# Kernel tuning notes

Measured on AMD Instinct MI355X. Metric: run time of the kernel, lower is better.

Reference implementation:

```python
import jax, jax.numpy as jnp
import numpy as np
import math

G = 256            # grid points per axis
L = 25.6           # cubic cell edge (bohr)
A = L / G          # grid spacing = 0.1 bohr
R_O = 2.0          # radial cutoff (bohr)
RMAX = int(math.ceil(R_O / A))   # 20
D = 2 * RMAX + 1                 # 41 box points per axis
N_ATOMS = 32
N_RAD = 4
N_L = 4
V_CELL = A ** 3
FOUR_PI = 4.0 * math.pi


def _make_W(n_rad):
    # NeuralXC ortho basis: S_ij = sqrt((5+2i)(5+2j))/(5+i+j), W = sqrtm(inv(S))
    i = np.arange(n_rad)
    S = np.sqrt((5.0 + 2 * i)[:, None] * (5.0 + 2 * i)[None, :]) / (5.0 + i[:, None] + i[None, :])
    w, V = np.linalg.eigh(np.linalg.inv(S))
    return (V * np.sqrt(w)) @ V.T


def setup_inputs():
    key = jax.random.key(0)
    k1, k2 = jax.random.split(key)
    rho = jax.random.uniform(k1, (G, G, G), dtype=jnp.float32)
    positions = jax.random.uniform(k2, (N_ATOMS, 3), dtype=jnp.float32) * L
    W = jnp.asarray(_make_W(N_RAD), dtype=jnp.float32)
    # periodic mesh offsets: [0..RMAX, -RMAX..-1] as in mesh_3d
    offs = jnp.concatenate([jnp.arange(0, RMAX + 1), jnp.arange(-RMAX, 0)]).astype(jnp.int32)
    return {"rho": rho, "positions": positions, "W": W, "offs": offs}


def _assoc_legendre(n_l, x, s):
    # P[l][m] for 0 <= m <= l < n_l, with Condon-Shortley phase
    P = [[None] * n_l for _ in range(n_l)]
    P[0][0] = jnp.ones_like(x)
    for m in range(n_l):
        if m > 0:
            P[m][m] = -(2 * m - 1) * s * P[m - 1][m - 1]
        if m + 1 < n_l:
            P[m + 1][m] = (2 * m + 1) * x * P[m][m]
        for l in range(m + 2, n_l):
            P[l][m] = ((2 * l - 1) * x * P[l - 1][m] - (l - 1 + m) * P[l - 2][m]) / (l - m)
    return P


def _real_sph_stack(n_l, theta, phi):
    # real spherical harmonics stacked in (l, m=-l..l) order -> [n_l**2, ...]
    x = jnp.cos(theta)
    s = jnp.sin(theta)
    P = _assoc_legendre(n_l, x, s)
    sq2 = math.sqrt(2.0)
    Ys = []
    for l in range(n_l):
        for m in range(-l, l + 1):
            am = abs(m)
            N = math.sqrt((2 * l + 1) / FOUR_PI * math.factorial(l - am) / math.factorial(l + am))
            if m == 0:
                Ys.append(N * P[l][0] * jnp.ones_like(x))
            elif m > 0:
                Ys.append(sq2 * ((-1) ** m) * N * P[l][m] * jnp.cos(m * phi))
            else:
                Ys.append(sq2 * ((-1) ** am) * N * P[l][am] * jnp.sin(am * phi))
    return jnp.stack(Ys)


def _radials(R, W):
    # g_a(r) = r^2 (r_o - r)^(a+2) / N_a for r < r_o, orthonormalized with W
    gs = []
    for a in range(N_RAD):
        Nn = math.sqrt(720.0 * R_O ** (11 + 2 * a) / float(np.prod([2 * a + k for k in range(5, 12)])))
        g = R ** 2 * (R_O - R) ** (a + 2) / Nn
        gs.append(jnp.where(R < R_O, g, 0.0))
    return jnp.einsum('nm,mxyz->nxyz', W, jnp.stack(gs))


def _project_atom(rho, pos, W, offs):
    cm = jnp.round(pos / A)                     # U_inv @ pos for diagonal cell
    dr = pos - A * cm
    idx = jnp.mod(offs[None, :] + cm.astype(jnp.int32)[:, None], G)   # [3, D] PBC mesh indices
    # separable irregular gather of the atom box (== torch rho[Xm,Ym,Zm] with fmod+negative-index wrap)
    srho = rho[idx[0][:, None, None], idx[1][None, :, None], idx[2][None, None, :]]  # [D,D,D]
    coord = A * offs.astype(jnp.float32)
    Xs = (coord - dr[0])[:, None, None]
    Ys = (coord - dr[1])[None, :, None]
    Zs = (coord - dr[2])[None, None, :]
    R = jnp.sqrt(Xs ** 2 + Ys ** 2 + Zs ** 2)   # [D,D,D]
    phi = jnp.arctan2(Ys, Xs)                   # [D,D,1], broadcasts
    small = R < 1e-15
    ratio = jnp.clip(jnp.where(small, 1.0, Zs / jnp.where(small, 1.0, R)), -1.0, 1.0)
    theta = jnp.where(small, 0.0, jnp.arccos(ratio))
    angs = _real_sph_stack(N_L, theta, phi)     # [N_L**2, D,D,D]
    rads = _radials(R, W) * V_CELL              # [N_RAD,  D,D,D]
    # equals the original padded 'lmijk,nijk,ijk->nlm' einsum followed by selecting |m|<=l,
    # flattened in (n, l, m) order
    coeff = jnp.einsum('cxyz,nxyz,xyz->nc', angs, rads, srho)
    return coeff.reshape(-1)                    # [N_RAD * N_L**2]


def reference(rho, positions, W, offs):
    return jax.vmap(lambda p: _project_atom(rho, p, W, offs))(positions)  # [N_ATOMS, 64]
```

## Files before the change

### kernel.cpp

```cpp
#include <hip/hip_runtime.h>
#include <math.h>

#define G 256
#define NATOMS 32
#define RC2I 435
#define NCHUNK 16

typedef float f32x2 __attribute__((ext_vector_type(2)));

struct PMap {
    int n;
    unsigned int pts[40960];
};

constexpr PMap make_pmap() {
    PMap m{};
    int p = 0;
    for (int i = 0; i < 41; ++i) {
        int di = i - 20;
        int mi = RC2I - di * di;
        for (int j = 0; j < 41; ++j) {
            int dj = j - 20;
            int mj = mi - dj * dj;
            if (mj >= 0) {
                int h = 0;
                while ((h + 1) * (h + 1) <= mj) ++h;
                for (int k = 20 - h; k <= 20 + h; ++k)
                    m.pts[p++] = (unsigned)(i | (j << 8) | (k << 16));
            }
        }
    }
    m.n = p;
    return m;
}

constexpr PMap h_pmap = make_pmap();
constexpr int NPTS = h_pmap.n;
__device__ const PMap d_pmap = h_pmap;

__global__ __launch_bounds__(256, 2) void proj_kernel(
    const float* __restrict__ rho,
    const float* __restrict__ positions,
    const float* __restrict__ W,
    float* __restrict__ out,
    float cs0, float cs1, float cs2, float cs3)
{
    const int atom = blockIdx.y;
    const int chunk = blockIdx.x;
    const int tid = threadIdx.x;
    const float A = 0.1f;

    __shared__ float red[256];

    float px = positions[atom * 3 + 0];
    float py = positions[atom * 3 + 1];
    float pz = positions[atom * 3 + 2];
    float cmx = rintf(px / A), cmy = rintf(py / A), cmz = rintf(pz / A);
    float drx = px - A * cmx, dry = py - A * cmy, drz = pz - A * cmz;
    int cxi = (int)cmx, cyi = (int)cmy, czi = (int)cmz;

    const int cxo = (cxi - 20) & 255;
    const int cyo = (cyi - 20) & 255;
    const int czo = (czi - 20) & 255;
    const float xoff = -2.0f - drx;
    const float yoff = -2.0f - dry;
    const float zoff = -2.0f - drz;

    const int pbeg = (chunk * NPTS) / NCHUNK;
    const int pend = ((chunk + 1) * NPTS) / NCHUNK;
    const unsigned int* __restrict__ pts = d_pmap.pts;

    f32x2 acc2[32];
#pragma unroll
    for (int q = 0; q < 32; ++q) acc2[q] = (f32x2){0.0f, 0.0f};

    for (int p = pbeg + tid; p < pend; p += 256) {
        unsigned pr = pts[p];
        int ii = pr & 255;
        int dj = (pr >> 8) & 255;
        int dk = pr >> 16;
        float srho = rho[(((ii + cxo) & 255) << 16) |
                         (((dj + cyo) & 255) << 8) |
                         ((dk + czo) & 255)];
        float Xd = fmaf(A, (float)ii, xoff);
        float Yd = fmaf(A, (float)dj, yoff);
        float Zd = fmaf(A, (float)dk, zoff);

        float r2 = fmaf(Xd, Xd, fmaf(Yd, Yd, Zd * Zd));
        float invr = rsqrtf(fmaxf(r2, 1e-24f));
        float r = r2 * invr;
        float t = fmaxf(2.0f - r, 0.0f);
        float tt = t * t;
        float rs = r2 * srho;
        float g0 = rs * tt, g1 = g0 * t, g2 = g1 * t, g3 = g2 * t;
        float rv[4] = {g0, g1, g2, g3};

        float xr = Xd * invr, yr = Yd * invr, zr = Zd * invr;
        float xx = xr * xr, yy = yr * yr, zz = zr * zr;
        float xy = xr * yr, yz = yr * zr, xz = xr * zr;
        float xmy = xx - yy;
        float q51 = fmaf(5.0f, zz, -1.0f);
        f32x2 Y[8];
        Y[0] = (f32x2){0.28209479177387814f, 0.4886025119029199f * yr};
        Y[1] = (f32x2){0.4886025119029199f * zr, 0.4886025119029199f * xr};
        Y[2] = (f32x2){1.0925484305920792f * xy, 1.0925484305920792f * yz};
        Y[3] = (f32x2){0.31539156525252005f * fmaf(3.0f, zz, -1.0f),
                       1.0925484305920792f * xz};
        Y[4] = (f32x2){0.5462742152960396f * xmy,
                       0.5900435899266435f * yr * fmaf(3.0f, xx, -yy)};
        Y[5] = (f32x2){2.890611442640554f * xy * zr,
                       0.4570457994644658f * yr * q51};
        Y[6] = (f32x2){0.3731763325901154f * zr * fmaf(5.0f, zz, -3.0f),
                       0.4570457994644658f * xr * q51};
        Y[7] = (f32x2){1.445305721320277f * zr * xmy,
                       0.5900435899266435f * xr * fmaf(xx, 1.0f, -3.0f * yy)};

#pragma unroll
        for (int a = 0; a < 4; ++a) {
            f32x2 s = {rv[a], rv[a]};
#pragma unroll
            for (int q = 0; q < 8; ++q)
                acc2[a * 8 + q] = __builtin_elementwise_fma(s, Y[q], acc2[a * 8 + q]);
        }
    }

    float av[64];
#pragma unroll
    for (int q = 0; q < 32; ++q) { av[2 * q] = acc2[q].x; av[2 * q + 1] = acc2[q].y; }

    int lane = tid & 63;
#pragma unroll
    for (int s = 0; s < 6; ++s) {
        int d = 1 << s;
        bool hi = (lane & d) != 0;
#pragma unroll
        for (int pp = 0; pp < (64 >> (s + 1)); ++pp) {
            float send = hi ? av[2 * pp] : av[2 * pp + 1];
            float recv = __shfl_xor(send, d, 64);
            float keep = hi ? av[2 * pp + 1] : av[2 * pp];
            av[pp] = keep + recv;
        }
    }

    int wave = tid >> 6;
    red[wave * 64 + lane] = av[0];
    __syncthreads();
    if (tid < 64) {
        float s = red[tid] + red[64 + tid] + red[128 + tid] + red[192 + tid];
        int c = tid & 15;
        float m0 = __shfl(s, c, 64);
        float m1 = __shfl(s, 16 + c, 64);
        float m2 = __shfl(s, 32 + c, 64);
        float m3 = __shfl(s, 48 + c, 64);
        int n = tid >> 4;
        float v = fmaf(W[n * 4 + 3] * cs3, m3,
                  fmaf(W[n * 4 + 2] * cs2, m2,
                  fmaf(W[n * 4 + 1] * cs1, m1,
                       W[n * 4 + 0] * cs0 * m0)));
        atomicAdd(&out[atom * 64 + tid], v);
    }
}

extern "C" void kernel_launch(void* const* d_in, const int* in_sizes, int n_in,
                              void* d_out, int out_size, void* d_ws, size_t ws_size,
                              hipStream_t stream) {
    const float* rho = (const float*)d_in[0];
    const float* positions = (const float*)d_in[1];
    const float* W = (const float*)d_in[2];
    float* out = (float*)d_out;

    double Ad = 25.6 / 256.0;
    double vcell = Ad * Ad * Ad;
    float cs[4];
    for (int a = 0; a < 4; ++a) {
        double prod = 1.0;
        for (int k = 5; k < 12; ++k) prod *= (double)(2 * a + k);
        double nn = sqrt(720.0 * pow(2.0, 11 + 2 * a) / prod);
        cs[a] = (float)(vcell / nn);
    }

    dim3 grid(NCHUNK, NATOMS);
    proj_kernel<<<grid, 256, 0, stream>>>(rho, positions, W, out,
                                          cs[0], cs[1], cs[2], cs[3]);
}
```

Measured before the change: 101.8 us.

## Software-prefetch next gather, pack wrapped index math, raise grid and occupancy

The point loop is software-pipelined so the next point's packed index and rho gather are issued before the current point's math runs, hiding gather latency. The packed point encoding is reordered (k in the low byte, i in the high byte) so the wrapped address comes from two masked SWAR adds instead of three separate shift/mask/add sequences. The chunk count goes from 16 to 24 and launch bounds from 2 to 3 blocks per SIMD, adding parallelism at the cost of register pressure on the 64 accumulators. The first prefetch reads pts[pbeg+tid] even when that thread has no work. It stays inside the table, but it adds one redundant load.

```diff
diff --git a/kernel.cpp b/kernel.cpp
--- a/kernel.cpp
+++ b/kernel.cpp
@@ -4,7 +4,7 @@
 #define G 256
 #define NATOMS 32
 #define RC2I 435
-#define NCHUNK 16
+#define NCHUNK 24
 
 typedef float f32x2 __attribute__((ext_vector_type(2)));
 
@@ -26,7 +26,7 @@
                 int h = 0;
                 while ((h + 1) * (h + 1) <= mj) ++h;
                 for (int k = 20 - h; k <= 20 + h; ++k)
-                    m.pts[p++] = (unsigned)(i | (j << 8) | (k << 16));
+                    m.pts[p++] = (unsigned)(k | (j << 8) | (i << 16));
             }
         }
     }
@@ -38,7 +38,7 @@
 constexpr int NPTS = h_pmap.n;
 __device__ const PMap d_pmap = h_pmap;
 
-__global__ __launch_bounds__(256, 2) void proj_kernel(
+__global__ __launch_bounds__(256, 3) void proj_kernel(
     const float* __restrict__ rho,
     const float* __restrict__ positions,
     const float* __restrict__ W,
@@ -59,9 +59,11 @@
     float drx = px - A * cmx, dry = py - A * cmy, drz = pz - A * cmz;
     int cxi = (int)cmx, cyi = (int)cmy, czi = (int)cmz;
 
-    const int cxo = (cxi - 20) & 255;
-    const int cyo = (cyi - 20) & 255;
-    const int czo = (czi - 20) & 255;
+    const unsigned cxo = (unsigned)((cxi - 20) & 255);
+    const unsigned cyo = (unsigned)((cyi - 20) & 255);
+    const unsigned czo = (unsigned)((czi - 20) & 255);
+    const unsigned eoff = czo | (cxo << 16);
+    const unsigned ooff = cyo << 8;
     const float xoff = -2.0f - drx;
     const float yoff = -2.0f - dry;
     const float zoff = -2.0f - drz;
@@ -74,14 +76,21 @@
 #pragma unroll
     for (int q = 0; q < 32; ++q) acc2[q] = (f32x2){0.0f, 0.0f};
 
-    for (int p = pbeg + tid; p < pend; p += 256) {
-        unsigned pr = pts[p];
-        int ii = pr & 255;
-        int dj = (pr >> 8) & 255;
-        int dk = pr >> 16;
-        float srho = rho[(((ii + cxo) & 255) << 16) |
-                         (((dj + cyo) & 255) << 8) |
-                         ((dk + czo) & 255)];
+    int p = pbeg + tid;
+    unsigned pr = pts[p];
+    float srho = rho[(((pr & 0x00FF00FFu) + eoff) & 0x00FF00FFu) |
+                     (((pr & 0x0000FF00u) + ooff) & 0x0000FF00u)];
+
+    while (p < pend) {
+        int pn = p + 256;
+        int pl = pn < pend ? pn : p;
+        unsigned prn = pts[pl];
+        float srhon = rho[(((prn & 0x00FF00FFu) + eoff) & 0x00FF00FFu) |
+                          (((prn & 0x0000FF00u) + ooff) & 0x0000FF00u)];
+
+        int ii = (int)(pr >> 16);
+        int dj = (int)((pr >> 8) & 255u);
+        int dk = (int)(pr & 255u);
         float Xd = fmaf(A, (float)ii, xoff);
         float Yd = fmaf(A, (float)dj, yoff);
         float Zd = fmaf(A, (float)dk, zoff);
@@ -122,6 +131,10 @@
             for (int q = 0; q < 8; ++q)
                 acc2[a * 8 + q] = __builtin_elementwise_fma(s, Y[q], acc2[a * 8 + q]);
         }
+
+        pr = prn;
+        srho = srhon;
+        p = pn;
     }
 
     float av[64];
```

Result: faster. 97.10 us (-4.7%).
